# Kernel optimization log

Hardware: AMD Instinct MI355X
Metric: run time of the kernel (lower is better)

Reference implementation:

```python
import jax, jax.numpy as jnp
from jax import lax
import numpy as np

N, I, O = 64, 8, 8
B = 512
S_EX, S_PHI, S_RHO = 10, 60, 60  # S_phi must equal S_rho (alpha loops feed S_rho-sized h into the GRUs)
N_ACTIONS, N_ROLES = 5, 7


def _gru(x, h, Wih, Whh, bih, bhh):
    # torch.nn.GRUCell math
    gi = x @ Wih.T + bih
    gh = h @ Whh.T + bhh
    ir, iz, inn = jnp.split(gi, 3, axis=-1)
    hr, hz, hn = jnp.split(gh, 3, axis=-1)
    r = jax.nn.sigmoid(ir + hr)
    zg = jax.nn.sigmoid(iz + hz)
    n = jnp.tanh(inn + r * hn)
    return (1.0 - zg) * n + zg * h


def setup_inputs() -> dict:
    key = jax.random.key(0)
    ks = jax.random.split(key, 24)
    f32 = jnp.float32
    z = jax.random.normal(ks[0], (B, N, S_EX), f32)
    dz = jax.random.normal(ks[1], (B, N, S_EX), f32)
    has = (jax.random.uniform(ks[2], (B, N)) < 0.9).astype(f32)
    adj = (jnp.triu(jax.random.uniform(ks[3], (N, N)), 1) > 0.7).astype(jnp.int32)

    def lin(k, o, i):
        return (jax.random.normal(k, (o, i), f32) * np.float32(1.0 / np.sqrt(i)))

    d = dict(z=z, dz=dz, has=has, adj=adj)
    d['Wih_f'] = lin(ks[4], 3 * S_PHI, S_RHO)
    d['Whh_f'] = lin(ks[5], 3 * S_PHI, S_PHI)
    d['bih_f'] = jax.random.normal(ks[6], (3 * S_PHI,), f32) * 0.02
    d['bhh_f'] = jax.random.normal(ks[7], (3 * S_PHI,), f32) * 0.02
    d['Wih_b'] = lin(ks[8], 3 * S_PHI, S_RHO)
    d['Whh_b'] = lin(ks[9], 3 * S_PHI, S_PHI)
    d['bih_b'] = jax.random.normal(ks[10], (3 * S_PHI,), f32) * 0.02
    d['bhh_b'] = jax.random.normal(ks[11], (3 * S_PHI,), f32) * 0.02
    d['Wf'] = lin(ks[12], S_RHO, S_PHI + 2 * S_EX)
    d['bf'] = jax.random.normal(ks[13], (S_RHO,), f32) * 0.02
    d['Wb'] = lin(ks[14], S_RHO, S_PHI + 2 * S_EX)
    d['bb'] = jax.random.normal(ks[15], (S_RHO,), f32) * 0.02
    d['Wa'] = lin(ks[16], N_ACTIONS, 2 * S_PHI)
    d['ba'] = jax.random.normal(ks[17], (N_ACTIONS,), f32) * 0.02
    d['Wc'] = lin(ks[18], 1, 2 * S_PHI)
    d['bc'] = jax.random.normal(ks[19], (1,), f32) * 0.02
    d['Wu'] = lin(ks[20], N_ROLES, 2 * S_RHO)
    d['bu'] = jax.random.normal(ks[21], (N_ROLES,), f32) * 0.02
    return d


def reference(z, dz, has, adj,
              Wih_f, Whh_f, bih_f, bhh_f,
              Wih_b, Whh_b, bih_b, bhh_b,
              Wf, bf, Wb, bb, Wa, ba, Wc, bc, Wu, bu):
    Bn, Nn = has.shape
    dt = z.dtype
    adjf = adj.astype(dt)

    # ---- forward sweep over nodes in ascending order ----
    def fwd_outer(rho, i):
        def inner(h, j):
            hn = _gru(rho[j], h, Wih_f, Whh_f, bih_f, bhh_f)
            blend = adjf[j, i] * has[:, j][:, None]  # edge exists AND source node present
            return h + blend * (hn - h), None
        h, _ = lax.scan(inner, jnp.zeros((Bn, S_PHI), dt), jnp.arange(Nn))
        rho_i = jnp.tanh(jnp.concatenate([h, z[:, i], dz[:, i]], 1) @ Wf.T + bf)
        return rho.at[i].set(rho_i), None

    rho_f, _ = lax.scan(fwd_outer, jnp.zeros((Nn, Bn, S_RHO), dt), jnp.arange(Nn))

    # ---- backward sweep over nodes in descending order ----
    def bwd_outer(rho, i):
        def inner(h, j):
            hn = _gru(rho[j], h, Wih_b, Whh_b, bih_b, bhh_b)
            blend = adjf[i, j] * has[:, j][:, None]  # out-edges of i, visited descending
            return h + blend * (hn - h), None
        h, _ = lax.scan(inner, jnp.zeros((Bn, S_PHI), dt), jnp.arange(Nn - 1, -1, -1))
        rho_i = jnp.concatenate([h, z[:, i], dz[:, i]], 1) @ Wb.T + bb
        return rho.at[i].set(rho_i), None

    rho_b, _ = lax.scan(bwd_outer, jnp.zeros((Nn, Bn, S_RHO), dt), jnp.arange(Nn - 1, -1, -1))

    # ---- aggregate outputs (last O nodes) and inputs (first I nodes) ----
    h = jnp.zeros((Bn, S_RHO), dt)
    for i in range(N - O, N):
        hn = _gru(rho_f[i], h, Wih_f, Whh_f, bih_f, bhh_f)
        h = h + has[:, i][:, None] * (hn - h)
    alpha_f = h
    h = jnp.zeros((Bn, S_RHO), dt)
    for i in reversed(range(I)):
        hn = _gru(rho_b[i], h, Wih_b, Whh_b, bih_b, bhh_b)
        h = h + has[:, i][:, None] * (hn - h)
    alpha_b = h

    ab = jnp.concatenate([alpha_f, alpha_b], 1)
    omega = ab @ Wa.T + ba          # [B, 5]
    value = ab @ Wc.T + bc          # [B, 1]

    feats = jnp.concatenate([rho_f, rho_b], -1)           # [N, B, 2*S_rho]
    psi = jnp.einsum('nbs,rs->brn', feats, Wu) + bu[None, :, None]  # [B, 7, N]
    m = has[:, None, :]
    psi = -60.0 * (1.0 - m) + psi * m  # interpolate(-60, psi, has)

    instr_prob = jax.nn.softmax(omega, axis=1)
    role_prob = jax.nn.softmax(psi, axis=2)
    return instr_prob, role_prob, value
```

## Files before the change

### kernel.cpp

```cpp
#include <hip/hip_runtime.h>
#include <hip/hip_bf16.h>

#define NN 64
#define BATCH 512
#define SP 60
#define SG 180
#define SEX 10
#define CATD 80
#define NA 5
#define NR 7
#define OO 8
#define II 8

typedef unsigned long long u64;
typedef unsigned short u16;
typedef unsigned int u32;
typedef unsigned char u8;

#define OFF_Z     0
#define OFF_DZ    327680
#define OFF_HAS   655360
#define OFF_WIHF  688128
#define OFF_WHHF  698928
#define OFF_BIHF  709728
#define OFF_BHHF  709908
#define OFF_WIHB  710088
#define OFF_WHHB  720888
#define OFF_BIHB  731688
#define OFF_BHHB  731868
#define OFF_WF    732048
#define OFF_BF    736848
#define OFF_WB    736908
#define OFF_BB    741708
#define OFF_WA    741768
#define OFF_BA    742368
#define OFF_WC    742373
#define OFF_BC    742493
#define OFF_WU    742494
#define OFF_BU    743334
#define CONV_TOTAL 743341
#define OFF_FLAG  743342
#define OFF_RHOF  743344
#define OFF_RHOB  (OFF_RHOF + 1966080)
#define OFF_ALF   (OFF_RHOB + 1966080)
#define OFF_ALB   (OFF_ALF + 30720)
#define OUT_TOTAL 232448

typedef _Float16 f16;
typedef _Float16 half2_t __attribute__((ext_vector_type(2)));
typedef _Float16 f16x8 __attribute__((ext_vector_type(8)));
typedef float f32x4 __attribute__((ext_vector_type(4)));

__device__ __forceinline__ float us2f(u16 v){
  return __uint_as_float(((u32)v) << 16);
}
__device__ __forceinline__ u16 f2bf(float f){
  __hip_bfloat16 h = __float2bfloat16(f);
  return *reinterpret_cast<u16*>(&h);
}
__device__ __forceinline__ float rcp_(float x){ return __builtin_amdgcn_rcpf(x); }
__device__ __forceinline__ float sigm(float x){
  return rcp_(1.f + __expf(-x));
}
__device__ __forceinline__ float tanh_(float x){
  float e = __expf(2.f*fabsf(x));
  float t = 1.f - 2.f*rcp_(e + 1.f);
  return copysignf(t, x);
}
__device__ __forceinline__ u32 pack2(float a, float b){
  half2_t h; h[0] = (f16)a; h[1] = (f16)b;
  return __builtin_bit_cast(u32, h);
}
__device__ __forceinline__ float fdot2_(u32 a, u32 b, float c){
  return __builtin_amdgcn_fdot2(__builtin_bit_cast(half2_t, a),
                                __builtin_bit_cast(half2_t, b), c, false);
}
__device__ __forceinline__ f16x8 bc16(uint4 v){ return __builtin_bit_cast(f16x8, v); }
__device__ __forceinline__ f32x4 mfma16(f16x8 a, f16x8 b, f32x4 c){
  return __builtin_amdgcn_mfma_f32_16x16x32_f16(a, b, c, 0, 0, 0);
}

__device__ __forceinline__ int detect_bf16(const u32* w){
  int f = 0;
  for (int i=0;i<256;i++) f |= (w[i] == 0x3F803F80u) ? 1 : 0;
  return f;
}

__global__ __launch_bounds__(256) void conv_in(
  const void* z, const void* dz, const void* has,
  const void* WihF, const void* WhhF, const void* bihF, const void* bhhF,
  const void* WihB, const void* WhhB, const void* bihB, const void* bhhB,
  const void* Wf_, const void* bf_, const void* Wb_, const void* bb_,
  const void* Wa, const void* ba, const void* Wc, const void* bc,
  const void* Wu, const void* bu, float* ws)
{
  const int isbf = detect_bf16((const u32*)has);
  if (blockIdx.x == 0 && threadIdx.x == 0) ws[OFF_FLAG] = (float)isbf;
  int idx = blockIdx.x*256 + threadIdx.x;
  if (idx >= CONV_TOTAL) return;
  const void* src; int loc;
  if      (idx < OFF_DZ  ){ src=z;    loc=idx-OFF_Z;    }
  else if (idx < OFF_HAS ){ src=dz;   loc=idx-OFF_DZ;   }
  else if (idx < OFF_WIHF){ src=has;  loc=idx-OFF_HAS;  }
  else if (idx < OFF_WHHF){ src=WihF; loc=idx-OFF_WIHF; }
  else if (idx < OFF_BIHF){ src=WhhF; loc=idx-OFF_WHHF; }
  else if (idx < OFF_BHHF){ src=bihF; loc=idx-OFF_BIHF; }
  else if (idx < OFF_WIHB){ src=bhhF; loc=idx-OFF_BHHF; }
  else if (idx < OFF_WHHB){ src=WihB; loc=idx-OFF_WIHB; }
  else if (idx < OFF_BIHB){ src=WhhB; loc=idx-OFF_WHHB; }
  else if (idx < OFF_BHHB){ src=bihB; loc=idx-OFF_BIHB; }
  else if (idx < OFF_WF  ){ src=bhhB; loc=idx-OFF_BHHB; }
  else if (idx < OFF_BF  ){ src=Wf_;  loc=idx-OFF_WF;   }
  else if (idx < OFF_WB  ){ src=bf_;  loc=idx-OFF_BF;   }
  else if (idx < OFF_BB  ){ src=Wb_;  loc=idx-OFF_WB;   }
  else if (idx < OFF_WA  ){ src=bb_;  loc=idx-OFF_BB;   }
  else if (idx < OFF_BA  ){ src=Wa;   loc=idx-OFF_WA;   }
  else if (idx < OFF_WC  ){ src=ba;   loc=idx-OFF_BA;   }
  else if (idx < OFF_BC  ){ src=Wc;   loc=idx-OFF_WC;   }
  else if (idx < OFF_WU  ){ src=bc;   loc=idx-OFF_BC;   }
  else if (idx < OFF_BU  ){ src=Wu;   loc=idx-OFF_WU;   }
  else                    { src=bu;   loc=idx-OFF_BU;   }
  float v = isbf ? us2f(((const u16*)src)[loc]) : ((const float*)src)[loc];
  ws[idx] = v;
}

__global__ __launch_bounds__(256, 4) void dir_kernel(const int* __restrict__ adj,
                                                     float* __restrict__ ws)
{
  const int tid = threadIdx.x;
  const int w   = tid >> 6;
  const int u   = tid & 63;
  const int ml  = u & 15;
  const int q   = u >> 4;
  const int bid = blockIdx.x;
  const int bwd = bid >> 9;
  const int b   = bid & 511;

  const float* Wih  = ws + (bwd ? OFF_WIHB : OFF_WIHF);
  const float* Whh  = ws + (bwd ? OFF_WHHB : OFF_WHHF);
  const float* bih  = ws + (bwd ? OFF_BIHB : OFF_BIHF);
  const float* bhh  = ws + (bwd ? OFF_BHHB : OFF_BHHF);
  const float* Wcat = ws + (bwd ? OFF_WB   : OFF_WF);
  const float* bcat = ws + (bwd ? OFF_BB   : OFF_BF);
  const float* zc   = ws + OFF_Z;
  const float* dzc  = ws + OFF_DZ;
  const float* hasc = ws + OFF_HAS;
  float* rho   = ws + (bwd ? OFF_RHOB : OFF_RHOF);
  float* alpha = ws + (bwd ? OFF_ALB  : OFF_ALF);

  __shared__ uint4 sH4[65][9];
  __shared__ uint4 sRhoHist[8][8];
  __shared__ float sZdc[NN][SP];
  __shared__ float sPart[4][64];
  __shared__ u32 sZp[NN][5];
  __shared__ u32 sDZp[NN][5];
  __shared__ float sHas[NN];
  __shared__ u64 sRowM[NN];
  __shared__ u8 sConsL[NN][64];
  __shared__ int sConsCnt[NN];

  #define ROWB(I) ((char*)&sH4[(I)][0])
  const u32 BIASW = 0x3C000000u;

  {
    if (tid < 64){
      u64 rowm = 0;
      for (int j=0;j<64;j++) rowm |= ((u64)(adj[tid*64+j]!=0))<<j;
      sRowM[tid] = rowm;
      sHas[tid] = hasc[b*NN + tid];
    }
    for (int idx=tid; idx<65*9; idx+=256){
      uint4 v = {0,0,0,0};
      if (idx % 9 == 7) v.w = BIASW;
      ((uint4*)sH4)[idx] = v;
    }
    if (tid < 64){ uint4 v={0,0,0,0}; if ((tid&7)==7) v.w = BIASW; ((uint4*)sRhoHist)[tid]=v; }
    for (int idx=tid; idx<NN*5; idx+=256){
      int n2=idx/5, p2=idx%5;
      sZp [n2][p2] = pack2(zc [(size_t)b*NN*SEX + n2*SEX + 2*p2],
                           zc [(size_t)b*NN*SEX + n2*SEX + 2*p2+1]);
      sDZp[n2][p2] = pack2(dzc[(size_t)b*NN*SEX + n2*SEX + 2*p2],
                           dzc[(size_t)b*NN*SEX + n2*SEX + 2*p2+1]);
    }
  }
  __syncthreads();
  if (tid < 64){
    u64 cm = 0;
    if (bwd) for (int i2=0;i2<64;i2++) cm |= ((sRowM[i2]>>tid)&1ULL)<<i2;
    u64 m = bwd ? cm : sRowM[tid];
    int c = 0;
    while (m){ int i2 = (int)__builtin_ctzll(m); m &= m-1; sConsL[tid][c++] = (u8)i2; }
    sConsCnt[tid] = c;
  }
  {
    const int uu = tid & 63;
    const int tw = tid >> 6;
    if (uu < SP){
      u32 wz[10];
      #pragma unroll
      for (int p=0;p<10;p++)
        wz[p] = pack2(Wcat[uu*CATD + 60 + 2*p], Wcat[uu*CATD + 60 + 2*p + 1]);
      const float bb0 = bcat[uu];
      for (int t2=tw; t2<NN; t2+=4){
        float c = bb0;
        #pragma unroll
        for (int p=0;p<5;p++){
          c = fdot2_(wz[p],   sZp [t2][p], c);
          c = fdot2_(wz[5+p], sDZp[t2][p], c);
        }
        sZdc[t2][uu] = c;
      }
    }
  }

  f16x8 Ar[4], Az[4], Anh[2], Ani[2];
  {
    const int R = 16*w + ml;
    const bool rok = (R < SP);
    #pragma unroll
    for (int kt=0; kt<4; kt++){
      f16x8 vr, vz;
      #pragma unroll
      for (int j=0;j<8;j++){
        const int K = 32*kt + 8*q + j;
        float wr=0.f, wz2=0.f;
        if (rok){
          if (K < SP){ wr = Whh[R*SP+K]; wz2 = Whh[(60+R)*SP+K]; }
          else if (K >= 64 && K < 64+SP){ wr = Wih[R*SP+(K-64)]; wz2 = Wih[(60+R)*SP+(K-64)]; }
          else if (K == 127){ wr = bhh[R]+bih[R]; wz2 = bhh[60+R]+bih[60+R]; }
        }
        vr[j]=(f16)wr; vz[j]=(f16)wz2;
      }
      Ar[kt]=vr; Az[kt]=vz;
    }
    #pragma unroll
    for (int kt=0; kt<2; kt++){
      f16x8 vn, vi;
      #pragma unroll
      for (int j=0;j<8;j++){
        const int K = 32*kt + 8*q + j;
        float wn=0.f, wi=0.f;
        if (rok){
          if (K < SP){ wn = Whh[(120+R)*SP+K]; wi = Wih[(120+R)*SP+K]; }
          else if (K == 63){ wn = bhh[120+R]; wi = bih[120+R]; }
        }
        vn[j]=(f16)wn; vi[j]=(f16)wi;
      }
      Anh[kt]=vn; Ani[kt]=vi;
    }
  }

  u32 wc[8];
  #pragma unroll
  for (int k=0;k<8;k++){
    const int kk = 8*w + k;
    wc[k] = (kk < 30) ? pack2(Wcat[u*CATD + 2*kk], Wcat[u*CATD + 2*kk + 1]) : 0u;
  }
  __syncthreads();

  auto gates = [&](f32x4 Dr, f32x4 Dz, f32x4 Dn, f32x4 Gn,
                   int ci, bool wr, float bl){
    char* rp = ROWB(ci) + 32*w + 8*q;
    uint2 h2 = *(uint2*)rp;
    half2_t ha = __builtin_bit_cast(half2_t, h2.x);
    half2_t hb = __builtin_bit_cast(half2_t, h2.y);
    float hold[4] = { (float)ha[0], (float)ha[1], (float)hb[0], (float)hb[1] };
    float hw[4];
    #pragma unroll
    for (int reg=0;reg<4;reg++){
      float r_ = sigm(Dr[reg]);
      float zg = sigm(Dz[reg]);
      float nv = tanh_(Gn[reg] + r_*Dn[reg]);
      float hn_ = (1.f - zg)*nv + zg*hold[reg];
      hw[reg] = (bl != 0.f) ? hn_ : hold[reg];
    }
    if (wr && !(w==3 && q==3)){
      uint2 o; o.x = pack2(hw[0],hw[1]); o.y = pack2(hw[2],hw[3]);
      *(uint2*)rp = o;
    }
  };

  auto fullpass = [&](f16x8 Bh0, f16x8 Bh1, f16x8 Br0, f16x8 Br1,
                      f32x4 Gn, int ci, bool wr, float bl){
    f32x4 Dr={0,0,0,0}, Dz={0,0,0,0}, Dn={0,0,0,0};
    Dr = mfma16(Ar[0], Bh0, Dr); Dr = mfma16(Ar[1], Bh1, Dr);
    Dr = mfma16(Ar[2], Br0, Dr); Dr = mfma16(Ar[3], Br1, Dr);
    Dz = mfma16(Az[0], Bh0, Dz); Dz = mfma16(Az[1], Bh1, Dz);
    Dz = mfma16(Az[2], Br0, Dz); Dz = mfma16(Az[3], Br1, Dz);
    Dn = mfma16(Anh[0], Bh0, Dn); Dn = mfma16(Anh[1], Bh1, Dn);
    gates(Dr, Dz, Dn, Gn, ci, wr, bl);
  };

  int t = bwd ? 63 : 0;
  const int dt = bwd ? -1 : 1;
  for (int s=0; s<64; s++, t+=dt){
    const float blendT = sHas[t];
    const int cnt = sConsCnt[t];
    const bool act = (blendT != 0.f) && (cnt > 0);

    f32x4 Dr={0,0,0,0}, Dz={0,0,0,0}, Dn={0,0,0,0};
    int ci0 = 64;
    if (act){
      ci0 = (ml < cnt) ? (int)sConsL[t][ml] : 64;
      const f16x8 Bh0 = bc16(sH4[ci0][q]);
      const f16x8 Bh1 = bc16(sH4[ci0][4+q]);
      Dr = mfma16(Ar[0], Bh0, Dr); Dr = mfma16(Ar[1], Bh1, Dr);
      Dz = mfma16(Az[0], Bh0, Dz); Dz = mfma16(Az[1], Bh1, Dz);
      Dn = mfma16(Anh[0], Bh0, Dn); Dn = mfma16(Anh[1], Bh1, Dn);
    }

    {
      const uint4* hr = &sH4[t][0];
      uint4 ha = hr[2*w];
      uint4 hb = hr[2*w+1];
      float cA = 0.f;
      float cB = (w == 3) ? ((u < SP) ? sZdc[t][u] : 0.f) : 0.f;
      cA = fdot2_(wc[0], ha.x, cA); cB = fdot2_(wc[1], ha.y, cB);
      cA = fdot2_(wc[2], ha.z, cA); cB = fdot2_(wc[3], ha.w, cB);
      cA = fdot2_(wc[4], hb.x, cA); cB = fdot2_(wc[5], hb.y, cB);
      if (w < 3){ cA = fdot2_(wc[6], hb.z, cA); cB = fdot2_(wc[7], hb.w, cB); }
      sPart[w][u] = cA + cB;
    }
    __syncthreads();

    float acc = (sPart[0][u] + sPart[1][u]) + (sPart[2][u] + sPart[3][u]);
    float rv = bwd ? acc : tanh_(acc);
    if (w == 0){
      if (u < SP) rho[((size_t)t*BATCH + b)*SP + u] = rv;
      const int slot = bwd ? t : (t - (NN-OO));
      if (slot >= 0 && slot < 8 && u < SP)
        *(f16*)((char*)&sRhoHist[slot][0] + 2*u) = (f16)rv;
    }

    if (act){
      const float rvm = (u < SP) ? rv : ((u == 63) ? 1.f : 0.f);
      const int rvb = __builtin_bit_cast(int, rvm);
      uint4 B0, B1;
      {
        u32 w0[4], w1[4];
        #pragma unroll
        for (int j=0;j<4;j++){
          const int i0 = (8*q + 2*j)*4;
          int a0 = __builtin_amdgcn_ds_bpermute(i0,     rvb);
          int a1 = __builtin_amdgcn_ds_bpermute(i0+4,   rvb);
          int c0 = __builtin_amdgcn_ds_bpermute(i0+128, rvb);
          int c1 = __builtin_amdgcn_ds_bpermute(i0+132, rvb);
          w0[j] = pack2(__builtin_bit_cast(float,a0), __builtin_bit_cast(float,a1));
          w1[j] = pack2(__builtin_bit_cast(float,c0), __builtin_bit_cast(float,c1));
        }
        B0.x=w0[0]; B0.y=w0[1]; B0.z=w0[2]; B0.w=w0[3];
        B1.x=w1[0]; B1.y=w1[1]; B1.z=w1[2]; B1.w=w1[3];
      }
      const f16x8 Br0 = bc16(B0);
      const f16x8 Br1 = bc16(B1);

      f32x4 Gn={0,0,0,0};
      Gn = mfma16(Ani[0], Br0, Gn);
      Gn = mfma16(Ani[1], Br1, Gn);

      Dr = mfma16(Ar[2], Br0, Dr); Dr = mfma16(Ar[3], Br1, Dr);
      Dz = mfma16(Az[2], Br0, Dz); Dz = mfma16(Az[3], Br1, Dz);
      gates(Dr, Dz, Dn, Gn, ci0, ml < cnt, 1.0f);

      if (cnt > 16){
        const int idxp = 16 + ml;
        const int ci = (idxp < cnt) ? (int)sConsL[t][idxp] : 64;
        const f16x8 Bh0 = bc16(sH4[ci][q]);
        const f16x8 Bh1 = bc16(sH4[ci][4+q]);
        fullpass(Bh0, Bh1, Br0, Br1, Gn, ci, idxp < cnt, 1.0f);
      }
    }
    __syncthreads();
  }

  for (int s2=0; s2<8; s2++){
    const int i = bwd ? (7 - s2) : (NN - OO + s2);
    const int slot = bwd ? i : (i - (NN-OO));
    const f16x8 Th0 = bc16(sH4[64][q]);
    const f16x8 Th1 = bc16(sH4[64][4+q]);
    const f16x8 Tr0 = bc16(sRhoHist[slot][q]);
    const f16x8 Tr1 = bc16(sRhoHist[slot][4+q]);
    f32x4 Gt={0,0,0,0};
    Gt = mfma16(Ani[0], Tr0, Gt);
    Gt = mfma16(Ani[1], Tr1, Gt);
    __syncthreads();
    fullpass(Th0, Th1, Tr0, Tr1, Gt, 64, ml==0, sHas[i]);
    __syncthreads();
  }
  if (tid < SP) alpha[(size_t)b*SP + tid] = (float)*(const f16*)(ROWB(64) + 2*tid);
  #undef ROWB
}

__global__ __launch_bounds__(256, 1) void head_kernel(float* __restrict__ ws,
                                                      void* __restrict__ outp)
{
  const int b = blockIdx.x;
  const int tid = threadIdx.x;
  const int isbf = (ws[OFF_FLAG] != 0.f);
  const float* hasc   = ws + OFF_HAS;
  const float* WaC    = ws + OFF_WA;
  const float* baC    = ws + OFF_BA;
  const float* WcC    = ws + OFF_WC;
  const float* bcC    = ws + OFF_BC;
  const float* WuC    = ws + OFF_WU;
  const float* buC    = ws + OFF_BU;
  const float* rhoF   = ws + OFF_RHOF;
  const float* rhoB   = ws + OFF_RHOB;
  const float* alphaF = ws + OFF_ALF;
  const float* alphaB = ws + OFF_ALB;

  __shared__ float sF[NN][121];
  __shared__ float sAB[120];
  __shared__ float sWu[NR*120];
  __shared__ float sHasR[NN];
  __shared__ float sPsi[NR][NN];
  __shared__ float sRed[NR][2];
  __shared__ float sOm[NA];

  auto wout = [&](int idx, float v){
    if (isbf) ((u16*)outp)[idx] = f2bf(v);
    else      ((float*)outp)[idx] = v;
  };

  for (int idx=tid; idx<NN*SP; idx+=256){
    int n = idx/SP, s = idx%SP;
    sF[n][s]    = rhoF[((size_t)n*BATCH + b)*SP + s];
    sF[n][60+s] = rhoB[((size_t)n*BATCH + b)*SP + s];
  }
  for (int idx=tid; idx<120; idx+=256)
    sAB[idx] = (idx<60) ? alphaF[(size_t)b*SP + idx] : alphaB[(size_t)b*SP + idx-60];
  for (int idx=tid; idx<NR*120; idx+=256) sWu[idx] = WuC[idx];
  for (int idx=tid; idx<NN; idx+=256) sHasR[idx] = hasc[b*NN + idx];
  __syncthreads();

  for (int idx=tid; idx<NR*NN; idx+=256){
    int r = idx/NN, n = idx%NN;
    float acc = buC[r];
    for (int s=0;s<120;s++) acc += sF[n][s]*sWu[r*120+s];
    sPsi[r][n] = (sHasR[n] != 0.f) ? acc : -60.f;
  }
  if (tid >= 64 && tid < 64+NA){
    int a = tid - 64;
    float acc = baC[a];
    for (int s=0;s<120;s++) acc += sAB[s]*WaC[a*120+s];
    sOm[a] = acc;
  }
  if (tid == 70){
    float acc = bcC[0];
    for (int s=0;s<120;s++) acc += sAB[s]*WcC[s];
    wout(2560 + BATCH*NR*NN + b, acc);
  }
  __syncthreads();

  if (tid < NR){
    float m = -1e30f;
    for (int n=0;n<NN;n++) m = fmaxf(m, sPsi[tid][n]);
    float ssum = 0.f;
    for (int n=0;n<NN;n++) ssum += __expf(sPsi[tid][n]-m);
    sRed[tid][0] = m; sRed[tid][1] = 1.f/ssum;
  }
  if (tid == 8){
    float m = -1e30f;
    for (int a=0;a<NA;a++) m = fmaxf(m, sOm[a]);
    float e[NA]; float ssum = 0.f;
    for (int a=0;a<NA;a++){ e[a] = __expf(sOm[a]-m); ssum += e[a]; }
    for (int a=0;a<NA;a++) wout(b*NA + a, e[a]/ssum);
  }
  __syncthreads();

  for (int idx=tid; idx<NR*NN; idx+=256){
    int r = idx/NN, n = idx%NN;
    float v = __expf(sPsi[r][n]-sRed[r][0]) * sRed[r][1];
    wout(2560 + (size_t)b*NR*NN + idx, v);
  }
}

extern "C" void kernel_launch(void* const* d_in, const int* in_sizes, int n_in,
                              void* d_out, int out_size, void* d_ws, size_t ws_size,
                              hipStream_t stream)
{
  const int* adj = (const int*)d_in[3];
  float* ws = (float*)d_ws;

  conv_in<<<(CONV_TOTAL+255)/256, 256, 0, stream>>>(
      d_in[0], d_in[1], d_in[2],
      d_in[4], d_in[5], d_in[6], d_in[7],
      d_in[8], d_in[9], d_in[10], d_in[11],
      d_in[12], d_in[13], d_in[14], d_in[15],
      d_in[16], d_in[17], d_in[18], d_in[19],
      d_in[20], d_in[21], ws);

  dir_kernel<<<1024, 256, 0, stream>>>(adj, ws);

  head_kernel<<<512, 256, 0, stream>>>(ws, d_out);
}
```

Before: 291.4 us.

## Hoist second consumer group hidden MFMAs before barrier, stage rho via LDS

The hidden-state MFMAs for the second group of up to 16 consumers now run before the per-step barrier, so they overlap the rho reduction instead of running after it. The ds_bpermute gather that built the rho B-operand in every wave is replaced: wave 0 writes rho as f16 into a small padded LDS buffer, and every wave reads it back after an added __syncthreads. A loop now handles consumer groups beyond 32, which the earlier code did not process. The trade-off is an extra block barrier per step and more live accumulator registers.

```diff
diff --git a/kernel.cpp b/kernel.cpp
--- a/kernel.cpp
+++ b/kernel.cpp
@@ -149,6 +149,7 @@
   float* alpha = ws + (bwd ? OFF_ALB  : OFF_ALF);
 
   __shared__ uint4 sH4[65][9];
+  __shared__ uint4 sRhoPad[8];
   __shared__ uint4 sRhoHist[8][8];
   __shared__ float sZdc[NN][SP];
   __shared__ float sPart[4][64];
@@ -174,6 +175,7 @@
       if (idx % 9 == 7) v.w = BIASW;
       ((uint4*)sH4)[idx] = v;
     }
+    if (tid < 8){ uint4 v={0,0,0,0}; if (tid==7) v.w = BIASW; sRhoPad[tid]=v; }
     if (tid < 64){ uint4 v={0,0,0,0}; if ((tid&7)==7) v.w = BIASW; ((uint4*)sRhoHist)[tid]=v; }
     for (int idx=tid; idx<NN*5; idx+=256){
       int n2=idx/5, p2=idx%5;
@@ -297,9 +299,11 @@
     const float blendT = sHas[t];
     const int cnt = sConsCnt[t];
     const bool act = (blendT != 0.f) && (cnt > 0);
+    const bool g1  = act && (cnt > 16);
 
     f32x4 Dr={0,0,0,0}, Dz={0,0,0,0}, Dn={0,0,0,0};
-    int ci0 = 64;
+    f32x4 Dr2={0,0,0,0}, Dz2={0,0,0,0}, Dn2={0,0,0,0};
+    int ci0 = 64, ci1 = 64;
     if (act){
       ci0 = (ml < cnt) ? (int)sConsL[t][ml] : 64;
       const f16x8 Bh0 = bc16(sH4[ci0][q]);
@@ -307,6 +311,14 @@
       Dr = mfma16(Ar[0], Bh0, Dr); Dr = mfma16(Ar[1], Bh1, Dr);
       Dz = mfma16(Az[0], Bh0, Dz); Dz = mfma16(Az[1], Bh1, Dz);
       Dn = mfma16(Anh[0], Bh0, Dn); Dn = mfma16(Anh[1], Bh1, Dn);
+      if (g1){
+        ci1 = (16 + ml < cnt) ? (int)sConsL[t][16 + ml] : 64;
+        const f16x8 Ch0 = bc16(sH4[ci1][q]);
+        const f16x8 Ch1 = bc16(sH4[ci1][4+q]);
+        Dr2 = mfma16(Ar[0], Ch0, Dr2); Dr2 = mfma16(Ar[1], Ch1, Dr2);
+        Dz2 = mfma16(Az[0], Ch0, Dz2); Dz2 = mfma16(Az[1], Ch1, Dz2);
+        Dn2 = mfma16(Anh[0], Ch0, Dn2); Dn2 = mfma16(Anh[1], Ch1, Dn2);
+      }
     }
 
     {
@@ -323,37 +335,22 @@
     }
     __syncthreads();
 
-    float acc = (sPart[0][u] + sPart[1][u]) + (sPart[2][u] + sPart[3][u]);
-    float rv = bwd ? acc : tanh_(acc);
     if (w == 0){
-      if (u < SP) rho[((size_t)t*BATCH + b)*SP + u] = rv;
+      float acc = (sPart[0][u] + sPart[1][u]) + (sPart[2][u] + sPart[3][u]);
+      float rv = bwd ? acc : tanh_(acc);
+      if (u < SP){
+        rho[((size_t)t*BATCH + b)*SP + u] = rv;
+        *(f16*)((char*)&sRhoPad[0] + 2*u) = (f16)rv;
+      }
       const int slot = bwd ? t : (t - (NN-OO));
       if (slot >= 0 && slot < 8 && u < SP)
         *(f16*)((char*)&sRhoHist[slot][0] + 2*u) = (f16)rv;
     }
+    __syncthreads();
 
     if (act){
-      const float rvm = (u < SP) ? rv : ((u == 63) ? 1.f : 0.f);
-      const int rvb = __builtin_bit_cast(int, rvm);
-      uint4 B0, B1;
-      {
-        u32 w0[4], w1[4];
-        #pragma unroll
-        for (int j=0;j<4;j++){
-          const int i0 = (8*q + 2*j)*4;
-          int a0 = __builtin_amdgcn_ds_bpermute(i0,     rvb);
-          int a1 = __builtin_amdgcn_ds_bpermute(i0+4,   rvb);
-          int c0 = __builtin_amdgcn_ds_bpermute(i0+128, rvb);
-          int c1 = __builtin_amdgcn_ds_bpermute(i0+132, rvb);
-          w0[j] = pack2(__builtin_bit_cast(float,a0), __builtin_bit_cast(float,a1));
-          w1[j] = pack2(__builtin_bit_cast(float,c0), __builtin_bit_cast(float,c1));
-        }
-        B0.x=w0[0]; B0.y=w0[1]; B0.z=w0[2]; B0.w=w0[3];
-        B1.x=w1[0]; B1.y=w1[1]; B1.z=w1[2]; B1.w=w1[3];
-      }
-      const f16x8 Br0 = bc16(B0);
-      const f16x8 Br1 = bc16(B1);
-
+      const f16x8 Br0 = bc16(sRhoPad[q]);
+      const f16x8 Br1 = bc16(sRhoPad[4+q]);
       f32x4 Gn={0,0,0,0};
       Gn = mfma16(Ani[0], Br0, Gn);
       Gn = mfma16(Ani[1], Br1, Gn);
@@ -362,8 +359,14 @@
       Dz = mfma16(Az[2], Br0, Dz); Dz = mfma16(Az[3], Br1, Dz);
       gates(Dr, Dz, Dn, Gn, ci0, ml < cnt, 1.0f);
 
-      if (cnt > 16){
-        const int idxp = 16 + ml;
+      if (g1){
+        Dr2 = mfma16(Ar[2], Br0, Dr2); Dr2 = mfma16(Ar[3], Br1, Dr2);
+        Dz2 = mfma16(Az[2], Br0, Dz2); Dz2 = mfma16(Az[3], Br1, Dz2);
+        gates(Dr2, Dz2, Dn2, Gn, ci1, 16 + ml < cnt, 1.0f);
+      }
+
+      for (int p=2; 16*p < cnt; p++){
+        const int idxp = 16*p + ml;
         const int ci = (idxp < cnt) ? (int)sConsL[t][idxp] : 64;
         const f16x8 Bh0 = bc16(sH4[ci][q]);
         const f16x8 Bh1 = bc16(sH4[ci][4+q]);
```

New measurement: 281.7 us. 3.3% less time.
